# Performance work log

Hardware: AMD Instinct MI355X
Metric: run time of the kernel (lower is better)

## Reference

```python
import jax, jax.numpy as jnp
import numpy as np

B = 4
P0, P1, P2 = 196608, 49152, 12288
DEG = 8
K = 4
EPS = 1e-5


def _cheb_conv(x, cols, vals, W, b):
    """Chebyshev graph conv. x: (B,P,Cin); cols/vals: (P,DEG) fixed-degree sparse L;
    W: (K*Cin, Cout); b: (Cout,). Recursion: T0=x, T1=Lx, Tk=2 L T_{k-1} - T_{k-2}."""
    def lmul(y):  # sparse matvec per batch/channel: (B,P,C) -> (B,P,C)
        return jnp.einsum('pd,bpdc->bpc', vals, y[:, cols, :])
    t0 = x
    t1 = lmul(t0)
    terms = [t0, t1]
    for _ in range(K - 2):
        t2 = 2.0 * lmul(t1) - t0
        terms.append(t2)
        t0, t1 = t1, t2
    xk = jnp.concatenate(terms, axis=-1)  # (B,P,K*Cin)
    return xk @ W + b


def _layernorm(h, g, bt):
    mu = jnp.mean(h, axis=-1, keepdims=True)
    var = jnp.mean(jnp.square(h - mu), axis=-1, keepdims=True)
    return g * (h - mu) / jnp.sqrt(var + EPS) + bt


def _avg_pool4(h):  # HEALPix nested-order average pooling: (B,P,C) -> (B,P//4,C)
    Bh, P, C = h.shape
    return h.reshape(Bh, P // 4, 4, C).mean(axis=2)


def setup_inputs() -> dict:
    key = jax.random.key(0)
    ks = jax.random.split(key, 16)
    cin, c1, c2, c3 = 16, 64, 128, 256
    hid, emb = 512, 256

    def glorot(k, shape):
        fan_in = shape[0]
        return jax.random.normal(k, shape, jnp.float32) / np.sqrt(fan_in)

    inp = {
        'x': jax.random.normal(ks[0], (B, P0, cin), jnp.float32),
        'cols1': jax.random.randint(ks[1], (P0, DEG), 0, P0),
        'vals1': 0.2 * jax.random.normal(ks[2], (P0, DEG), jnp.float32),
        'cols2': jax.random.randint(ks[3], (P1, DEG), 0, P1),
        'vals2': 0.2 * jax.random.normal(ks[4], (P1, DEG), jnp.float32),
        'cols3': jax.random.randint(ks[5], (P2, DEG), 0, P2),
        'vals3': 0.2 * jax.random.normal(ks[6], (P2, DEG), jnp.float32),
        'W1': glorot(ks[7], (K * cin, c1)), 'b1': jnp.zeros((c1,), jnp.float32),
        'g1': jnp.ones((c1,), jnp.float32), 'bt1': jnp.zeros((c1,), jnp.float32),
        'W2': glorot(ks[8], (K * c1, c2)), 'b2': jnp.zeros((c2,), jnp.float32),
        'g2': jnp.ones((c2,), jnp.float32), 'bt2': jnp.zeros((c2,), jnp.float32),
        'W3': glorot(ks[9], (K * c2, c3)), 'b3': jnp.zeros((c3,), jnp.float32),
        'g3': jnp.ones((c3,), jnp.float32), 'bt3': jnp.zeros((c3,), jnp.float32),
        'mW1': glorot(ks[10], (c3, hid)), 'mb1': jnp.zeros((hid,), jnp.float32),
        'mW2': glorot(ks[11], (hid, emb)), 'mb2': jnp.zeros((emb,), jnp.float32),
    }
    return inp


def reference(x, cols1, vals1, cols2, vals2, cols3, vals3,
              W1, b1, g1, bt1, W2, b2, g2, bt2, W3, b3, g3, bt3,
              mW1, mb1, mW2, mb2):
    # Stage 1: ChebConv -> LayerNorm -> ReLU -> avg pool (4:1)
    h = _cheb_conv(x, cols1, vals1, W1, b1)
    h = jax.nn.relu(_layernorm(h, g1, bt1))
    h = _avg_pool4(h)
    # Stage 2
    h = _cheb_conv(h, cols2, vals2, W2, b2)
    h = jax.nn.relu(_layernorm(h, g2, bt2))
    h = _avg_pool4(h)
    # Stage 3 (last stage: no pooling)
    h = _cheb_conv(h, cols3, vals3, W3, b3)
    h = jax.nn.relu(_layernorm(h, g3, bt3))
    # Global mean pool over pixels, then MLP head (Linear-ReLU-Linear)
    z = h.mean(axis=1)                     # (B, 256)
    z = jax.nn.relu(z @ mW1 + mb1)
    z = z @ mW2 + mb2                      # (B, 256)
    return z
```

## Files before the change

### kernel.cpp

```cpp
#include <hip/hip_runtime.h>
#include <hip/hip_bf16.h>

namespace {

constexpr int B  = 4;
constexpr int P0 = 196608, P1 = 49152, P2 = 12288;
constexpr int DEG = 8;
constexpr float EPS = 1e-5f;
constexpr int NBLK3 = (P2 * B) / 64;
constexpr int RSL = 16;
constexpr int RPB = NBLK3 / RSL;

typedef __attribute__((ext_vector_type(4))) float f32x4;
typedef __attribute__((ext_vector_type(8))) short s16x8;

__device__ __forceinline__ float b2f(unsigned short u) {
    union { unsigned int i; float f; } c; c.i = (unsigned int)u << 16; return c.f;
}
__device__ __forceinline__ unsigned short f2b(float f) {
    __hip_bfloat16 h = __float2bfloat16(f);
    return *reinterpret_cast<unsigned short*>(&h);
}

__global__ __launch_bounds__(256)
void x2p_kernel(const float* __restrict__ in, unsigned short* __restrict__ out)
{
    long idx = (long)blockIdx.x * blockDim.x + threadIdx.x;
    if (idx >= (long)P0 * B * 2) return;
    int  h = (int)(idx & 1);
    int  b = (int)((idx >> 1) & 3);
    long p = idx >> 3;
    const float* src = in + ((size_t)b * P0 + p) * 16 + h * 8;
    float4 v0 = *(const float4*)src;
    float4 v1 = *(const float4*)(src + 4);
    union { uint4 u; unsigned short s[8]; } o;
    o.s[0] = f2b(v0.x); o.s[1] = f2b(v0.y); o.s[2] = f2b(v0.z); o.s[3] = f2b(v0.w);
    o.s[4] = f2b(v1.x); o.s[5] = f2b(v1.y); o.s[6] = f2b(v1.z); o.s[7] = f2b(v1.w);
    *(uint4*)&out[((size_t)p * B + b) * 16 + h * 8] = o.u;
}

__global__ __launch_bounds__(256)
void wt_all_kernel(const float* __restrict__ W1, const float* __restrict__ W2,
                   const float* __restrict__ W3,
                   const float* __restrict__ mW1, const float* __restrict__ mW2,
                   unsigned short* __restrict__ Wt1, unsigned short* __restrict__ Wt2,
                   unsigned short* __restrict__ Wt3,
                   float* __restrict__ mW1t, float* __restrict__ mW2t)
{
    int i = blockIdx.x * 256 + threadIdx.x;
    if (i < 4096) {
        int n = i % 64, k = i / 64;
        Wt1[n * 64 + k] = f2b(W1[i]);
    } else if (i < 36864) {
        int j = i - 4096;
        int n = j % 128, k = j / 128;
        Wt2[n * 256 + k] = f2b(W2[j]);
    } else if (i < 167936) {
        int j = i - 36864;
        int n = j % 256, k = j / 256;
        Wt3[n * 512 + k] = f2b(W3[j]);
    } else if (i < 299008) {
        int j = i - 167936;
        int n = j % 512, k = j / 512;
        mW1t[(size_t)n * 256 + k] = mW1[j];
    } else if (i < 430080) {
        int j = i - 299008;
        int n = j % 256, k = j / 256;
        mW2t[(size_t)n * 512 + k] = mW2[j];
    }
}

template <int CV8>
__global__ __launch_bounds__(256)
void lmul_v2_kernel(const unsigned short* __restrict__ in,
                    const unsigned short* __restrict__ prev,
                    const int* __restrict__ cols, const float* __restrict__ vals,
                    unsigned short* __restrict__ out,
                    float alpha, float beta)
{
    constexpr int ROWS = 256 / CV8;
    __shared__ int   cs[ROWS * DEG];
    __shared__ float vs[ROWS * DEG];
    const int tid = threadIdx.x;
    const long r0 = (long)blockIdx.x * ROWS;
    if (tid < ROWS * DEG) {
        cs[tid] = cols[r0 * DEG + tid];
        vs[tid] = vals[r0 * DEG + tid];
    }
    __syncthreads();

    const int v  = tid & (CV8 - 1);
    const int lr = tid / CV8;
    const uint4* in16 = (const uint4*)in;

    float acc[8] = {0.f,0.f,0.f,0.f,0.f,0.f,0.f,0.f};
#pragma unroll
    for (int d = 0; d < DEG; ++d) {
        int   col = cs[lr * DEG + d];
        float w   = vs[lr * DEG + d];
        union { uint4 u; unsigned short s[8]; } x;
        x.u = in16[(size_t)col * CV8 + v];
#pragma unroll
        for (int j = 0; j < 8; ++j) acc[j] = fmaf(w, b2f(x.s[j]), acc[j]);
    }
    size_t o = (size_t)(r0 + lr) * CV8 + v;
    if (beta != 0.f) {
        union { uint4 u; unsigned short s[8]; } pv;
        pv.u = ((const uint4*)prev)[o];
#pragma unroll
        for (int j = 0; j < 8; ++j)
            acc[j] = fmaf(alpha, acc[j], beta * b2f(pv.s[j]));
    } else if (alpha != 1.f) {
#pragma unroll
        for (int j = 0; j < 8; ++j) acc[j] *= alpha;
    }
    union { uint4 u; unsigned short s[8]; } ou;
#pragma unroll
    for (int j = 0; j < 8; ++j) ou.s[j] = f2b(acc[j]);
    ((uint4*)out)[o] = ou.u;
}

__global__ __launch_bounds__(256)
void s1_mm_kernel(const unsigned short* __restrict__ t0,
                  const unsigned short* __restrict__ t1,
                  const unsigned short* __restrict__ t2,
                  const unsigned short* __restrict__ t3,
                  const unsigned short* __restrict__ Wt,
                  const float* __restrict__ bias,
                  const float* __restrict__ gam,
                  const float* __restrict__ bet,
                  unsigned short* __restrict__ out)
{
    const int wave = threadIdx.x >> 6;
    const int lane = threadIdx.x & 63;
    const int g    = lane >> 4;
    const int c16  = lane & 15;

    s16x8 wf[2][4];
#pragma unroll
    for (int ks = 0; ks < 2; ++ks)
#pragma unroll
        for (int n = 0; n < 4; ++n)
            wf[ks][n] = *(const s16x8*)&Wt[(size_t)(n * 16 + c16) * 64 + ks * 32 + g * 8];

    float bz[4], gz[4], tz[4];
#pragma unroll
    for (int n = 0; n < 4; ++n) {
        bz[n] = bias[n * 16 + c16];
        gz[n] = gam [n * 16 + c16];
        tz[n] = bet [n * 16 + c16];
    }

    const unsigned short* tb[4] = { t0, t1, t2, t3 };
    const int term0  = g >> 1;
    const int coloff = (g & 1) * 8;
    const int bb     = c16 >> 2;
    const int px     = c16 & 3;

    constexpr int NT = P0 / 4;
    const int wg     = blockIdx.x * 4 + wave;
    const int wstep  = gridDim.x * 4;

    for (int t = wg; t < NT; t += wstep) {
        size_t rowbase = ((size_t)(t * 4 + px) * 4 + bb) * 16 + coloff;
        s16x8 a0 = *(const s16x8*)&tb[term0    ][rowbase];
        s16x8 a1 = *(const s16x8*)&tb[term0 + 2][rowbase];

        f32x4 acc[4];
#pragma unroll
        for (int n = 0; n < 4; ++n) acc[n] = (f32x4){bz[n], bz[n], bz[n], bz[n]};
#pragma unroll
        for (int n = 0; n < 4; ++n)
            acc[n] = __builtin_amdgcn_mfma_f32_16x16x32_bf16(a0, wf[0][n], acc[n], 0, 0, 0);
#pragma unroll
        for (int n = 0; n < 4; ++n)
            acc[n] = __builtin_amdgcn_mfma_f32_16x16x32_bf16(a1, wf[1][n], acc[n], 0, 0, 0);

        float s[4] = {0,0,0,0}, q[4] = {0,0,0,0};
#pragma unroll
        for (int n = 0; n < 4; ++n)
#pragma unroll
            for (int r = 0; r < 4; ++r) {
                float v = acc[n][r];
                s[r] += v; q[r] += v * v;
            }
#pragma unroll
        for (int msk = 1; msk < 16; msk <<= 1)
#pragma unroll
            for (int r = 0; r < 4; ++r) {
                s[r] += __shfl_xor(s[r], msk, 64);
                q[r] += __shfl_xor(q[r], msk, 64);
            }
        float mu[4], rs[4];
#pragma unroll
        for (int r = 0; r < 4; ++r) {
            mu[r] = s[r] * (1.f / 64.f);
            float var = q[r] * (1.f / 64.f) - mu[r] * mu[r];
            rs[r] = rsqrtf(var + EPS);
        }
        size_t ro = ((size_t)t * 4 + g) * 64;
#pragma unroll
        for (int n = 0; n < 4; ++n) {
            float pv = 0.f;
#pragma unroll
            for (int r = 0; r < 4; ++r) {
                float h = fmaf(gz[n] * rs[r], acc[n][r] - mu[r], tz[n]);
                pv += fmaxf(h, 0.f);
            }
            out[ro + n * 16 + c16] = f2b(pv * 0.25f);
        }
    }
}

template <int CIN, int COUT, int GM, int GN, int POOL, int LOG2CIN>
__global__ __launch_bounds__(512)
void cheb_mm_v3_kernel(const unsigned short* __restrict__ t0,
                       const unsigned short* __restrict__ t1,
                       const unsigned short* __restrict__ t2,
                       const unsigned short* __restrict__ t3,
                       const unsigned short* __restrict__ Wt,
                       const float* __restrict__ bias,
                       const float* __restrict__ gam,
                       const float* __restrict__ bet,
                       void* __restrict__ outv)
{
    constexpr int KC   = 4 * CIN;
    constexpr int BM   = GM * 64;
    constexpr int NKCH = KC / 64;

    __shared__ unsigned short As[BM * 64];
    __shared__ unsigned short Ws[COUT * 64];
    __shared__ float sq[BM][GN][2];

    const int tid  = threadIdx.x;
    const int wv   = tid >> 6;
    const int gm   = wv / GN;
    const int gn   = wv % GN;
    const int lane = tid & 63;
    const int g    = lane >> 4;
    const int c16  = lane & 15;

    const unsigned short* tb[4] = { t0, t1, t2, t3 };

    float bz[4], gz[4], tz[4];
#pragma unroll
    for (int n = 0; n < 4; ++n) {
        int col = gn * 64 + n * 16 + c16;
        bz[n] = bias[col]; gz[n] = gam[col]; tz[n] = bet[col];
    }

    f32x4 acc[4][4];
#pragma unroll
    for (int m = 0; m < 4; ++m)
#pragma unroll
        for (int n = 0; n < 4; ++n)
            acc[m][n] = (f32x4){bz[n], bz[n], bz[n], bz[n]};

    for (int kc = 0; kc < NKCH; ++kc) {
        if (kc) __syncthreads();
#pragma unroll
        for (int it = 0; it < BM * 8 / 512; ++it) {
            int i = tid + it * 512;
            int row = i >> 3, v = i & 7;
            int k = kc * 64 + v * 8;
            int term = k >> LOG2CIN;
            int c = k & (CIN - 1);
            size_t srow;
            if constexpr (POOL == 4) {
                int pix = blockIdx.x * (BM / 4) + ((row >> 4) << 2) + (row & 3);
                int rb  = (row >> 2) & 3;
                srow = ((size_t)pix * B + rb) * CIN + c;
            } else {
                srow = ((size_t)(blockIdx.x * BM + row)) * CIN + c;
            }
            *(uint4*)((char*)As + row * 128 + ((v * 16) ^ ((row & 7) << 4))) =
                *(const uint4*)&tb[term][srow];
        }
#pragma unroll
        for (int it = 0; it < COUT * 8 / 512; ++it) {
            int i = tid + it * 512;
            int co = i >> 3, v = i & 7;
            *(uint4*)((char*)Ws + co * 128 + ((v * 16) ^ ((co & 7) << 4))) =
                *(const uint4*)&Wt[(size_t)co * KC + kc * 64 + v * 8];
        }
        __syncthreads();
#pragma unroll
        for (int ks = 0; ks < 2; ++ks) {
            const int cb  = ks * 64 + g * 16;
            const int swz = cb ^ ((c16 & 7) << 4);
            s16x8 a[4], bw[4];
#pragma unroll
            for (int m = 0; m < 4; ++m)
                a[m] = *(const s16x8*)((const char*)As + (gm * 64 + m * 16 + c16) * 128 + swz);
#pragma unroll
            for (int n = 0; n < 4; ++n)
                bw[n] = *(const s16x8*)((const char*)Ws + (gn * 64 + n * 16 + c16) * 128 + swz);
#pragma unroll
            for (int n = 0; n < 4; ++n)
#pragma unroll
                for (int m = 0; m < 4; ++m)
                    acc[m][n] = __builtin_amdgcn_mfma_f32_16x16x32_bf16(a[m], bw[n], acc[m][n], 0, 0, 0);
        }
    }

    float sm[4][4], qm[4][4];
#pragma unroll
    for (int m = 0; m < 4; ++m)
#pragma unroll
        for (int r = 0; r < 4; ++r) { sm[m][r] = 0.f; qm[m][r] = 0.f; }
#pragma unroll
    for (int m = 0; m < 4; ++m)
#pragma unroll
        for (int n = 0; n < 4; ++n)
#pragma unroll
            for (int r = 0; r < 4; ++r) {
                float v = acc[m][n][r];
                sm[m][r] += v; qm[m][r] += v * v;
            }
#pragma unroll
    for (int msk = 1; msk < 16; msk <<= 1)
#pragma unroll
        for (int m = 0; m < 4; ++m)
#pragma unroll
            for (int r = 0; r < 4; ++r) {
                sm[m][r] += __shfl_xor(sm[m][r], msk, 64);
                qm[m][r] += __shfl_xor(qm[m][r], msk, 64);
            }
    __syncthreads();
    if (c16 == 0) {
#pragma unroll
        for (int m = 0; m < 4; ++m)
#pragma unroll
            for (int r = 0; r < 4; ++r) {
                sq[gm * 64 + m * 16 + g * 4 + r][gn][0] = sm[m][r];
                sq[gm * 64 + m * 16 + g * 4 + r][gn][1] = qm[m][r];
            }
    }
    __syncthreads();
    float mu[4][4], rs[4][4];
#pragma unroll
    for (int m = 0; m < 4; ++m)
#pragma unroll
        for (int r = 0; r < 4; ++r) {
            int row = gm * 64 + m * 16 + g * 4 + r;
            float ss = 0.f, qq = 0.f;
#pragma unroll
            for (int j = 0; j < GN; ++j) { ss += sq[row][j][0]; qq += sq[row][j][1]; }
            mu[m][r] = ss * (1.f / COUT);
            float var = qq * (1.f / COUT) - mu[m][r] * mu[m][r];
            rs[m][r] = rsqrtf(var + EPS);
        }

    if constexpr (POOL == 4) {
        unsigned short* outp = (unsigned short*)outv;
#pragma unroll
        for (int m = 0; m < 4; ++m) {
            size_t ro = ((size_t)(blockIdx.x * (BM / 16) + gm * 4 + m) * B + g) * COUT + gn * 64;
#pragma unroll
            for (int n = 0; n < 4; ++n) {
                float pv = 0.f;
#pragma unroll
                for (int r = 0; r < 4; ++r) {
                    float h = fmaf(gz[n] * rs[m][r], acc[m][n][r] - mu[m][r], tz[n]);
                    pv += fmaxf(h, 0.f);
                }
                outp[ro + n * 16 + c16] = f2b(pv * 0.25f);
            }
        }
    } else {
        float part[4][4];
#pragma unroll
        for (int n = 0; n < 4; ++n)
#pragma unroll
            for (int r = 0; r < 4; ++r) part[n][r] = 0.f;
#pragma unroll
        for (int m = 0; m < 4; ++m)
#pragma unroll
            for (int n = 0; n < 4; ++n)
#pragma unroll
                for (int r = 0; r < 4; ++r) {
                    float h = fmaf(gz[n] * rs[m][r], acc[m][n][r] - mu[m][r], tz[n]);
                    part[n][r] += fmaxf(h, 0.f);
                }
#pragma unroll
        for (int n = 0; n < 4; ++n)
#pragma unroll
            for (int r = 0; r < 4; ++r) {
                part[n][r] += __shfl_xor(part[n][r], 16, 64);
                part[n][r] += __shfl_xor(part[n][r], 32, 64);
            }
        if (g == 0) {
            float* zb = (float*)outv + ((size_t)(blockIdx.x * GM + gm)) * (B * COUT);
#pragma unroll
            for (int n = 0; n < 4; ++n)
#pragma unroll
                for (int r = 0; r < 4; ++r)
                    zb[(size_t)r * COUT + gn * 64 + n * 16 + c16] = part[n][r];
        }
    }
}

__global__ __launch_bounds__(256)
void zred_kernel(const float* __restrict__ zblk, float* __restrict__ zp2)
{
    int s   = blockIdx.x >> 2;
    int col = (blockIdx.x & 3) * 256 + threadIdx.x;
    float acc = 0.f;
#pragma unroll 8
    for (int r = 0; r < RPB; ++r)
        acc += zblk[(size_t)(s * RPB + r) * (B * 256) + col];
    zp2[(size_t)s * (B * 256) + col] = acc;
}

__global__ __launch_bounds__(256)
void headA_kernel(const float* __restrict__ zp2, const float* __restrict__ mW1t,
                  const float* __restrict__ mb1, float* __restrict__ hh)
{
    __shared__ float zs[B * 256];
    __shared__ float ph[256];
    const int tid = threadIdx.x;
    for (int idx = tid; idx < B * 256; idx += 256) {
        float s = 0.f;
#pragma unroll
        for (int sl = 0; sl < RSL; ++sl) s += zp2[(size_t)sl * (B * 256) + idx];
        zs[idx] = s * (1.f / P2);
    }
    __syncthreads();
    const int jl = tid & 31, b = (tid >> 5) & 3, ig = tid >> 7;
    const int j  = blockIdx.x * 32 + jl;
    const float4* wrow = (const float4*)&mW1t[(size_t)j * 256 + ig * 128];
    const float*  zb   = &zs[b * 256 + ig * 128];
    float acc = 0.f;
#pragma unroll
    for (int i4 = 0; i4 < 32; ++i4) {
        float4 wv = wrow[i4];
        acc += zb[i4*4]*wv.x + zb[i4*4+1]*wv.y + zb[i4*4+2]*wv.z + zb[i4*4+3]*wv.w;
    }
    ph[tid] = acc;
    __syncthreads();
    if (tid < 128) {
        float a = ph[tid] + ph[tid + 128] + mb1[j];
        hh[b * 512 + j] = fmaxf(a, 0.f);
    }
}

__global__ __launch_bounds__(256)
void headB_kernel(const float* __restrict__ hh, const float* __restrict__ mW2t,
                  const float* __restrict__ mb2, float* __restrict__ out)
{
    __shared__ float hs[B * 512];
    __shared__ float ph[256];
    const int tid = threadIdx.x;
    for (int idx = tid; idx < B * 512; idx += 256) hs[idx] = hh[idx];
    __syncthreads();
    const int cl = tid & 31, b = (tid >> 5) & 3, ig = tid >> 7;
    const int c  = blockIdx.x * 32 + cl;
    const float4* wrow = (const float4*)&mW2t[(size_t)c * 512 + ig * 256];
    const float*  hb   = &hs[b * 512 + ig * 256];
    float acc = 0.f;
#pragma unroll
    for (int j4 = 0; j4 < 64; ++j4) {
        float4 wv = wrow[j4];
        acc += hb[j4*4]*wv.x + hb[j4*4+1]*wv.y + hb[j4*4+2]*wv.z + hb[j4*4+3]*wv.w;
    }
    ph[tid] = acc;
    __syncthreads();
    if (tid < 128)
        out[b * 256 + c] = ph[tid] + ph[tid + 128] + mb2[c];
}

}

extern "C" void kernel_launch(void* const* d_in, const int* in_sizes, int n_in,
                              void* d_out, int out_size, void* d_ws, size_t ws_size,
                              hipStream_t stream)
{
    const float* x     = (const float*)d_in[0];
    const int*   cols1 = (const int*)  d_in[1];
    const float* vals1 = (const float*)d_in[2];
    const int*   cols2 = (const int*)  d_in[3];
    const float* vals2 = (const float*)d_in[4];
    const int*   cols3 = (const int*)  d_in[5];
    const float* vals3 = (const float*)d_in[6];
    const float* W1  = (const float*)d_in[7];
    const float* b1  = (const float*)d_in[8];
    const float* g1  = (const float*)d_in[9];
    const float* bt1 = (const float*)d_in[10];
    const float* W2  = (const float*)d_in[11];
    const float* b2  = (const float*)d_in[12];
    const float* g2  = (const float*)d_in[13];
    const float* bt2 = (const float*)d_in[14];
    const float* W3  = (const float*)d_in[15];
    const float* b3  = (const float*)d_in[16];
    const float* g3  = (const float*)d_in[17];
    const float* bt3 = (const float*)d_in[18];
    const float* mW1 = (const float*)d_in[19];
    const float* mb1 = (const float*)d_in[20];
    const float* mW2 = (const float*)d_in[21];
    const float* mb2 = (const float*)d_in[22];
    float* out = (float*)d_out;

    char* w = (char*)d_ws;
    size_t off = 0;
    auto alloc = [&](size_t bytes) -> void* {
        void* p = w + off;
        off += (bytes + 255) & ~(size_t)255;
        return p;
    };
    const size_t E1 = (size_t)B * P0 * 16;
    unsigned short* xb  = (unsigned short*)alloc(E1 * 2);
    unsigned short* t_a = (unsigned short*)alloc(E1 * 2);
    unsigned short* t_b = (unsigned short*)alloc(E1 * 2);
    unsigned short* t_c = (unsigned short*)alloc(E1 * 2);
    unsigned short* h1  = (unsigned short*)alloc((size_t)P1 * B * 64 * 2);
    unsigned short* h2  = (unsigned short*)alloc((size_t)P2 * B * 128 * 2);
    unsigned short* Wt1 = (unsigned short*)alloc(64 * 64 * 2);
    unsigned short* Wt2 = (unsigned short*)alloc(256 * 128 * 2);
    unsigned short* Wt3 = (unsigned short*)alloc(512 * 256 * 2);
    float*          mW1t = (float*)alloc((size_t)512 * 256 * 4);
    float*          mW2t = (float*)alloc((size_t)256 * 512 * 4);
    float*          zblk = (float*)alloc((size_t)NBLK3 * B * 256 * 4);
    float*          zp2  = (float*)alloc((size_t)RSL * B * 256 * 4);
    float*          hh   = (float*)alloc((size_t)B * 512 * 4);

    x2p_kernel<<<(int)(((long)P0 * B * 2 + 255) / 256), 256, 0, stream>>>(x, xb);
    wt_all_kernel<<<(430080 + 255) / 256, 256, 0, stream>>>(
        W1, W2, W3, mW1, mW2, Wt1, Wt2, Wt3, mW1t, mW2t);

    {
        lmul_v2_kernel<8><<<P0 / 32, 256, 0, stream>>>(xb,  nullptr, cols1, vals1, t_a, 1.f,  0.f);
        lmul_v2_kernel<8><<<P0 / 32, 256, 0, stream>>>(t_a, xb,      cols1, vals1, t_b, 2.f, -1.f);
        lmul_v2_kernel<8><<<P0 / 32, 256, 0, stream>>>(t_b, t_a,     cols1, vals1, t_c, 2.f, -1.f);
        s1_mm_kernel<<<2048, 256, 0, stream>>>(xb, t_a, t_b, t_c, Wt1, b1, g1, bt1, h1);
    }
    {
        lmul_v2_kernel<32><<<P1 / 8, 256, 0, stream>>>(h1,  nullptr, cols2, vals2, t_a, 1.f,  0.f);
        lmul_v2_kernel<32><<<P1 / 8, 256, 0, stream>>>(t_a, h1,      cols2, vals2, t_b, 2.f, -1.f);
        lmul_v2_kernel<32><<<P1 / 8, 256, 0, stream>>>(t_b, t_a,     cols2, vals2, t_c, 2.f, -1.f);
        cheb_mm_v3_kernel<64, 128, 4, 2, 4, 6><<<(P1 * B) / 256, 512, 0, stream>>>(
            h1, t_a, t_b, t_c, Wt2, b2, g2, bt2, h2);
    }
    {
        lmul_v2_kernel<64><<<P2 / 4, 256, 0, stream>>>(h2,  nullptr, cols3, vals3, t_a, 1.f,  0.f);
        lmul_v2_kernel<64><<<P2 / 4, 256, 0, stream>>>(t_a, h2,      cols3, vals3, t_b, 2.f, -1.f);
        lmul_v2_kernel<64><<<P2 / 4, 256, 0, stream>>>(t_b, t_a,     cols3, vals3, t_c, 2.f, -1.f);
        cheb_mm_v3_kernel<128, 256, 2, 4, 1, 7><<<(P2 * B) / 128, 512, 0, stream>>>(
            h2, t_a, t_b, t_c, Wt3, b3, g3, bt3, zblk);
    }
    zred_kernel<<<RSL * 4, 256, 0, stream>>>(zblk, zp2);
    headA_kernel<<<16, 256, 0, stream>>>(zp2, mW1t, mb1, hh);
    headB_kernel<<<8, 256, 0, stream>>>(hh, mW2t, mb2, out);

    (void)in_sizes; (void)n_in; (void)out_size; (void)ws_size;
}
```

Measured before the change: 407.2 us.

## Fold Chebyshev recursion into weights and register-prefetch GEMM tiles

Replaces the Chebyshev recurrence with plain powers of L (x, Lx, L²x, L³x) and folds the recurrence coefficients into the transformed weight matrices: T2 = 2L²x - x and T3 = 4L³x - 3Lx, so W0 -= W2, W1 -= 3W3, W2 *= 2, W3 *= 4. The sparse matvec kernels no longer read the previous term or apply alpha/beta, which removes one full tensor read per recursion step. The matmul kernel also prefetches the next K-chunk into registers while the current chunk is computed. Powers of L may grow in magnitude relative to Chebyshev terms and are stored in bf16, which can change numerical accuracy.

```diff
diff --git a/kernel.cpp b/kernel.cpp
--- a/kernel.cpp
+++ b/kernel.cpp
@@ -20,6 +20,17 @@
 __device__ __forceinline__ unsigned short f2b(float f) {
     __hip_bfloat16 h = __float2bfloat16(f);
     return *reinterpret_cast<unsigned short*>(&h);
+}
+
+__device__ __forceinline__ float chebw(const float* __restrict__ W,
+                                       int k, int n, int N, int Cin) {
+    int t = k / Cin, c = k - t * Cin;
+    float v = W[(size_t)k * N + n];
+    if (t == 0)      v = v - W[(size_t)(2 * Cin + c) * N + n];
+    else if (t == 1) v = v - 3.f * W[(size_t)(3 * Cin + c) * N + n];
+    else if (t == 2) v = 2.f * v;
+    else             v = 4.f * v;
+    return v;
 }
 
 __global__ __launch_bounds__(256)
@@ -50,15 +61,15 @@
     int i = blockIdx.x * 256 + threadIdx.x;
     if (i < 4096) {
         int n = i % 64, k = i / 64;
-        Wt1[n * 64 + k] = f2b(W1[i]);
+        Wt1[n * 64 + k] = f2b(chebw(W1, k, n, 64, 16));
     } else if (i < 36864) {
         int j = i - 4096;
         int n = j % 128, k = j / 128;
-        Wt2[n * 256 + k] = f2b(W2[j]);
+        Wt2[n * 256 + k] = f2b(chebw(W2, k, n, 128, 64));
     } else if (i < 167936) {
         int j = i - 36864;
         int n = j % 256, k = j / 256;
-        Wt3[n * 512 + k] = f2b(W3[j]);
+        Wt3[n * 512 + k] = f2b(chebw(W3, k, n, 256, 128));
     } else if (i < 299008) {
         int j = i - 167936;
         int n = j % 512, k = j / 512;
@@ -72,11 +83,9 @@
 
 template <int CV8>
 __global__ __launch_bounds__(256)
-void lmul_v2_kernel(const unsigned short* __restrict__ in,
-                    const unsigned short* __restrict__ prev,
+void lmul_v3_kernel(const unsigned short* __restrict__ in,
                     const int* __restrict__ cols, const float* __restrict__ vals,
-                    unsigned short* __restrict__ out,
-                    float alpha, float beta)
+                    unsigned short* __restrict__ out)
 {
     constexpr int ROWS = 256 / CV8;
     __shared__ int   cs[ROWS * DEG];
@@ -103,21 +112,10 @@
 #pragma unroll
         for (int j = 0; j < 8; ++j) acc[j] = fmaf(w, b2f(x.s[j]), acc[j]);
     }
-    size_t o = (size_t)(r0 + lr) * CV8 + v;
-    if (beta != 0.f) {
-        union { uint4 u; unsigned short s[8]; } pv;
-        pv.u = ((const uint4*)prev)[o];
-#pragma unroll
-        for (int j = 0; j < 8; ++j)
-            acc[j] = fmaf(alpha, acc[j], beta * b2f(pv.s[j]));
-    } else if (alpha != 1.f) {
-#pragma unroll
-        for (int j = 0; j < 8; ++j) acc[j] *= alpha;
-    }
     union { uint4 u; unsigned short s[8]; } ou;
 #pragma unroll
     for (int j = 0; j < 8; ++j) ou.s[j] = f2b(acc[j]);
-    ((uint4*)out)[o] = ou.u;
+    ((uint4*)out)[(size_t)(r0 + lr) * CV8 + v] = ou.u;
 }
 
 __global__ __launch_bounds__(256)
@@ -214,7 +212,7 @@
 
 template <int CIN, int COUT, int GM, int GN, int POOL, int LOG2CIN>
 __global__ __launch_bounds__(512)
-void cheb_mm_v3_kernel(const unsigned short* __restrict__ t0,
+void cheb_mm_v4_kernel(const unsigned short* __restrict__ t0,
                        const unsigned short* __restrict__ t1,
                        const unsigned short* __restrict__ t2,
                        const unsigned short* __restrict__ t3,
@@ -227,6 +225,8 @@
     constexpr int KC   = 4 * CIN;
     constexpr int BM   = GM * 64;
     constexpr int NKCH = KC / 64;
+    constexpr int AITS = BM * 8 / 512;
+    constexpr int WITS = COUT * 8 / 512;
 
     __shared__ unsigned short As[BM * 64];
     __shared__ unsigned short Ws[COUT * 64];
@@ -256,10 +256,11 @@
         for (int n = 0; n < 4; ++n)
             acc[m][n] = (f32x4){bz[n], bz[n], bz[n], bz[n]};
 
-    for (int kc = 0; kc < NKCH; ++kc) {
-        if (kc) __syncthreads();
-#pragma unroll
-        for (int it = 0; it < BM * 8 / 512; ++it) {
+    uint4 ra[AITS], rw[WITS];
+
+    auto load_chunk = [&](int kc) {
+#pragma unroll
+        for (int it = 0; it < AITS; ++it) {
             int i = tid + it * 512;
             int row = i >> 3, v = i & 7;
             int k = kc * 64 + v * 8;
@@ -273,17 +274,36 @@
             } else {
                 srow = ((size_t)(blockIdx.x * BM + row)) * CIN + c;
             }
-            *(uint4*)((char*)As + row * 128 + ((v * 16) ^ ((row & 7) << 4))) =
-                *(const uint4*)&tb[term][srow];
-        }
-#pragma unroll
-        for (int it = 0; it < COUT * 8 / 512; ++it) {
+            ra[it] = *(const uint4*)&tb[term][srow];
+        }
+#pragma unroll
+        for (int it = 0; it < WITS; ++it) {
             int i = tid + it * 512;
             int co = i >> 3, v = i & 7;
-            *(uint4*)((char*)Ws + co * 128 + ((v * 16) ^ ((co & 7) << 4))) =
-                *(const uint4*)&Wt[(size_t)co * KC + kc * 64 + v * 8];
-        }
+            rw[it] = *(const uint4*)&Wt[(size_t)co * KC + kc * 64 + v * 8];
+        }
+    };
+    auto write_chunk = [&]() {
+#pragma unroll
+        for (int it = 0; it < AITS; ++it) {
+            int i = tid + it * 512;
+            int row = i >> 3, v = i & 7;
+            *(uint4*)((char*)As + row * 128 + ((v * 16) ^ ((row & 7) << 4))) = ra[it];
+        }
+#pragma unroll
+        for (int it = 0; it < WITS; ++it) {
+            int i = tid + it * 512;
+            int co = i >> 3, v = i & 7;
+            *(uint4*)((char*)Ws + co * 128 + ((v * 16) ^ ((co & 7) << 4))) = rw[it];
+        }
+    };
+
+    load_chunk(0);
+    for (int kc = 0; kc < NKCH; ++kc) {
         __syncthreads();
+        write_chunk();
+        __syncthreads();
+        if (kc + 1 < NKCH) load_chunk(kc + 1);
 #pragma unroll
         for (int ks = 0; ks < 2; ++ks) {
             const int cb  = ks * 64 + g * 16;
@@ -528,23 +548,23 @@
         W1, W2, W3, mW1, mW2, Wt1, Wt2, Wt3, mW1t, mW2t);
 
     {
-        lmul_v2_kernel<8><<<P0 / 32, 256, 0, stream>>>(xb,  nullptr, cols1, vals1, t_a, 1.f,  0.f);
-        lmul_v2_kernel<8><<<P0 / 32, 256, 0, stream>>>(t_a, xb,      cols1, vals1, t_b, 2.f, -1.f);
-        lmul_v2_kernel<8><<<P0 / 32, 256, 0, stream>>>(t_b, t_a,     cols1, vals1, t_c, 2.f, -1.f);
+        lmul_v3_kernel<8><<<P0 / 32, 256, 0, stream>>>(xb,  cols1, vals1, t_a);
+        lmul_v3_kernel<8><<<P0 / 32, 256, 0, stream>>>(t_a, cols1, vals1, t_b);
+        lmul_v3_kernel<8><<<P0 / 32, 256, 0, stream>>>(t_b, cols1, vals1, t_c);
         s1_mm_kernel<<<2048, 256, 0, stream>>>(xb, t_a, t_b, t_c, Wt1, b1, g1, bt1, h1);
     }
     {
-        lmul_v2_kernel<32><<<P1 / 8, 256, 0, stream>>>(h1,  nullptr, cols2, vals2, t_a, 1.f,  0.f);
-        lmul_v2_kernel<32><<<P1 / 8, 256, 0, stream>>>(t_a, h1,      cols2, vals2, t_b, 2.f, -1.f);
-        lmul_v2_kernel<32><<<P1 / 8, 256, 0, stream>>>(t_b, t_a,     cols2, vals2, t_c, 2.f, -1.f);
-        cheb_mm_v3_kernel<64, 128, 4, 2, 4, 6><<<(P1 * B) / 256, 512, 0, stream>>>(
+        lmul_v3_kernel<32><<<P1 / 8, 256, 0, stream>>>(h1,  cols2, vals2, t_a);
+        lmul_v3_kernel<32><<<P1 / 8, 256, 0, stream>>>(t_a, cols2, vals2, t_b);
+        lmul_v3_kernel<32><<<P1 / 8, 256, 0, stream>>>(t_b, cols2, vals2, t_c);
+        cheb_mm_v4_kernel<64, 128, 4, 2, 4, 6><<<(P1 * B) / 256, 512, 0, stream>>>(
             h1, t_a, t_b, t_c, Wt2, b2, g2, bt2, h2);
     }
     {
-        lmul_v2_kernel<64><<<P2 / 4, 256, 0, stream>>>(h2,  nullptr, cols3, vals3, t_a, 1.f,  0.f);
-        lmul_v2_kernel<64><<<P2 / 4, 256, 0, stream>>>(t_a, h2,      cols3, vals3, t_b, 2.f, -1.f);
-        lmul_v2_kernel<64><<<P2 / 4, 256, 0, stream>>>(t_b, t_a,     cols3, vals3, t_c, 2.f, -1.f);
-        cheb_mm_v3_kernel<128, 256, 2, 4, 1, 7><<<(P2 * B) / 128, 512, 0, stream>>>(
+        lmul_v3_kernel<64><<<P2 / 4, 256, 0, stream>>>(h2,  cols3, vals3, t_a);
+        lmul_v3_kernel<64><<<P2 / 4, 256, 0, stream>>>(t_a, cols3, vals3, t_b);
+        lmul_v3_kernel<64><<<P2 / 4, 256, 0, stream>>>(t_b, cols3, vals3, t_c);
+        cheb_mm_v4_kernel<128, 256, 2, 4, 1, 7><<<(P2 * B) / 128, 512, 0, stream>>>(
             h2, t_a, t_b, t_c, Wt3, b3, g3, bt3, zblk);
     }
     zred_kernel<<<RSL * 4, 256, 0, stream>>>(zblk, zp2);
```

Measured after the change: 450.5 us. +10.6%, slower.
